# Kernel optimization log

Hardware: AMD Instinct MI355X
Metric: run time of the kernel (lower is better)

## Reference

```python
import jax, jax.numpy as jnp
import numpy as np

N_NODES = 150000       # original nodes
N_FRAG_NODES = 300000  # nodes duplicated across fragments
N_FRAGS = 30000        # number of fragments (segments of fragments_batch)
E = 1200000            # edges in combined fragment graph
D = 128                # nhid


def seg_mean(x, seg, num):
    s = jax.ops.segment_sum(x, seg, num_segments=num)
    c = jax.ops.segment_sum(jnp.ones((x.shape[0], 1), x.dtype), seg, num_segments=num)
    return s / jnp.maximum(c, 1.0)


def setup_inputs() -> dict:
    key = jax.random.key(0)
    ks = jax.random.split(key, 8)
    x = jax.random.normal(ks[0], (N_NODES, D), dtype=jnp.float32)
    mapper = jax.random.randint(ks[1], (N_FRAG_NODES,), 0, N_NODES)
    batch = jnp.sort(jax.random.randint(ks[2], (N_FRAG_NODES,), 0, N_FRAGS))
    edge_index = jax.random.randint(ks[3], (2, E), 0, N_FRAG_NODES)
    W_u = jax.random.normal(ks[4], (D, D), dtype=jnp.float32) * 0.05
    b_u = jnp.zeros((D,), dtype=jnp.float32)
    W_gcn = jax.random.normal(ks[5], (D, D), dtype=jnp.float32) * 0.05
    b_gcn = jnp.zeros((D,), dtype=jnp.float32)
    return {
        "x": x,
        "fragments_nodes_mapper": mapper,
        "fragments_batch": batch,
        "edge_index": edge_index,
        "W_u": W_u,
        "b_u": b_u,
        "W_gcn": W_gcn,
        "b_gcn": b_gcn,
        "i": 0,
    }


def gcn_conv(x, edge_index, W, b, n):
    # PyG GCNConv: add self loops, symmetric normalization D^-1/2 (A+I) D^-1/2, then linear.
    xw = x @ W  # [n, D]
    loops = jnp.arange(n, dtype=edge_index.dtype)
    row = jnp.concatenate([edge_index[0], loops])  # source
    col = jnp.concatenate([edge_index[1], loops])  # target (aggregation index)
    deg = jax.ops.segment_sum(jnp.ones(row.shape[0], x.dtype), col, num_segments=n)
    dinv = jnp.where(deg > 0, jax.lax.rsqrt(jnp.maximum(deg, 1.0)), 0.0)
    norm = dinv[row] * dinv[col]  # [E+n]
    msg = xw[row] * norm[:, None]
    out = jax.ops.segment_sum(msg, col, num_segments=n)
    return out + b


def reference(x, fragments_nodes_mapper, fragments_batch, edge_index, W_u, b_u, W_gcn, b_gcn, i):
    if i == 0:
        x = x[fragments_nodes_mapper]  # gather: [N_FRAG_NODES, D]
    # fragment-level mean pooling, broadcast back to fragment-nodes
    fragment = seg_mean(x, fragments_batch, N_FRAGS)[fragments_batch]
    # U[i-1]: MLP(nhid, nhid, nlayer=1, with_final_activation=True) -> Linear + ReLU
    x = x + jax.nn.relu(fragment @ W_u + b_u)
    # pool duplicated fragment-nodes back onto original nodes, then re-broadcast
    x = seg_mean(x, fragments_nodes_mapper, N_NODES)[fragments_nodes_mapper]
    # GCN over the combined fragment graph
    x = gcn_conv(x, edge_index, W_gcn, b_gcn, N_FRAG_NODES)
    fragment_x = seg_mean(x, fragments_batch, N_FRAGS)  # [N_FRAGS, D]
    return (fragment_x, x)
```

## Files before the change

kernel.cpp:

```cpp
#include <hip/hip_runtime.h>
#include <hip/hip_bf16.h>

#define N_NODES      150000
#define N_FRAG_NODES 300000
#define N_FRAGS      30000
#define NEDGE        1200000
#define NCNT         (N_NODES + N_FRAG_NODES)
#define D            128
#define DV           32
#define NX16         (N_NODES * 16)
#define SCAN_TILE    1024

typedef __attribute__((ext_vector_type(8))) short short8;
typedef __attribute__((ext_vector_type(8))) unsigned short u16x8;
typedef __attribute__((ext_vector_type(4))) float f32x4;
typedef __attribute__((ext_vector_type(2))) int i32x2;

__device__ __forceinline__ unsigned short f2bf(float f) {
    unsigned u = __float_as_uint(f);
    u = (u + 0x7FFFu + ((u >> 16) & 1u)) >> 16;
    return (unsigned short)u;
}
__device__ __forceinline__ float bf2f(unsigned short u) {
    return __uint_as_float((unsigned)u << 16);
}

__global__ void k_prep(const int* __restrict__ mapper, const int* __restrict__ batch,
                       const int* __restrict__ ecol, const float4* __restrict__ x4,
                       int* __restrict__ mcnt, int* __restrict__ ccnt,
                       int* __restrict__ startb, u16x8* __restrict__ x16) {
    int i = blockIdx.x * blockDim.x + threadIdx.x;
    if (i < NEDGE) atomicAdd(&ccnt[ecol[i]], 1);
    if (i < N_FRAG_NODES) atomicAdd(&mcnt[mapper[i]], 1);
    if (i <= N_FRAGS) {
        int lo = 0, hi = N_FRAG_NODES;
        while (lo < hi) { int mid = (lo + hi) >> 1; if (batch[mid] < i) lo = mid + 1; else hi = mid; }
        startb[i] = lo;
    }
    #pragma unroll
    for (int rep = 0; rep < 2; ++rep) {
        int slot = i + rep * NEDGE;
        if (slot < NX16) {
            float4 v0 = x4[(size_t)slot * 2];
            float4 v1 = x4[(size_t)slot * 2 + 1];
            u16x8 o;
            o[0] = f2bf(v0.x); o[1] = f2bf(v0.y); o[2] = f2bf(v0.z); o[3] = f2bf(v0.w);
            o[4] = f2bf(v1.x); o[5] = f2bf(v1.y); o[6] = f2bf(v1.z); o[7] = f2bf(v1.w);
            x16[slot] = o;
        }
    }
}

__global__ void k_scan_tile(const int* __restrict__ cnt, int* __restrict__ combst,
                            int* __restrict__ tsum) {
    __shared__ int buf[SCAN_TILE];
    int tid = threadIdx.x;
    int i = blockIdx.x * SCAN_TILE + tid;
    int v = (i < NCNT) ? cnt[i] : 0;
    buf[tid] = v;
    __syncthreads();
    for (int off = 1; off < SCAN_TILE; off <<= 1) {
        int t = (tid >= off) ? buf[tid - off] : 0;
        __syncthreads();
        buf[tid] += t;
        __syncthreads();
    }
    if (i < NCNT) combst[i] = buf[tid] - v;
    if (tid == SCAN_TILE - 1) tsum[blockIdx.x] = buf[tid];
}

__global__ void k_scan_tsum(int* __restrict__ tsum, int ntiles,
                            int* __restrict__ mstart, int* __restrict__ cstart) {
    __shared__ int buf[SCAN_TILE];
    int tid = threadIdx.x;
    int v = (tid < ntiles) ? tsum[tid] : 0;
    buf[tid] = v;
    __syncthreads();
    for (int off = 1; off < SCAN_TILE; off <<= 1) {
        int t = (tid >= off) ? buf[tid - off] : 0;
        __syncthreads();
        buf[tid] += t;
        __syncthreads();
    }
    if (tid < ntiles) tsum[tid] = buf[tid] - v;
    if (tid == SCAN_TILE - 1) {
        mstart[N_NODES] = N_FRAG_NODES;
        cstart[N_FRAG_NODES] = buf[tid] - N_FRAG_NODES;
    }
}

__global__ void k_scan_add(const int* __restrict__ combst, const int* __restrict__ tsum,
                           int* __restrict__ mstart, int* __restrict__ cstart,
                           const int* __restrict__ mapper, const int* __restrict__ cnt,
                           int2* __restrict__ sval) {
    int i = blockIdx.x * blockDim.x + threadIdx.x;
    if (i >= NCNT) return;
    int v = combst[i] + tsum[i >> 10];
    if (i < N_NODES) {
        mstart[i] = v;
    } else {
        int r = i - N_NODES;
        cstart[r] = v - N_FRAG_NODES;
        int2 s;
        s.x = mapper[r];
        s.y = __float_as_int(rsqrtf((float)(cnt[i] + 1)));
        sval[r] = s;
    }
}

__global__ void k_frag_mean(const u16x8* __restrict__ x16, const int* __restrict__ mapper,
                            const int* __restrict__ startb, u16x8* __restrict__ frag16) {
    int g = threadIdx.x >> 4, lane = threadIdx.x & 15;
    int b = blockIdx.x * 16 + g;
    if (b >= N_FRAGS) return;
    int s = startb[b], e = startb[b + 1];
    float a0[8], a1[8], a2[8], a3[8];
    #pragma unroll
    for (int j = 0; j < 8; ++j) { a0[j] = 0.f; a1[j] = 0.f; a2[j] = 0.f; a3[j] = 0.f; }
    int j = s;
    for (; j + 4 <= e; j += 4) {
        int m0 = mapper[j], m1 = mapper[j + 1], m2 = mapper[j + 2], m3 = mapper[j + 3];
        u16x8 v0 = x16[(size_t)m0 * 16 + lane];
        u16x8 v1 = x16[(size_t)m1 * 16 + lane];
        u16x8 v2 = x16[(size_t)m2 * 16 + lane];
        u16x8 v3 = x16[(size_t)m3 * 16 + lane];
        #pragma unroll
        for (int k = 0; k < 8; ++k) {
            a0[k] += bf2f(v0[k]); a1[k] += bf2f(v1[k]);
            a2[k] += bf2f(v2[k]); a3[k] += bf2f(v3[k]);
        }
    }
    for (; j < e; ++j) {
        int m0 = mapper[j];
        u16x8 v0 = x16[(size_t)m0 * 16 + lane];
        #pragma unroll
        for (int k = 0; k < 8; ++k) a0[k] += bf2f(v0[k]);
    }
    float c = (float)(e - s); if (c < 1.f) c = 1.f;
    float inv = 1.f / c;
    u16x8 r;
    #pragma unroll
    for (int k = 0; k < 8; ++k)
        r[k] = f2bf(((a0[k] + a1[k]) + (a2[k] + a3[k])) * inv);
    frag16[(size_t)b * 16 + lane] = r;
}

__global__ void k_build_wfrag(const float* __restrict__ W, short* __restrict__ wfrag) {
    int t = threadIdx.x;
    for (int e = t; e < 2048; e += 256) {
        int nt = e >> 8;
        int kk = (e >> 6) & 3;
        int lane = e & 63;
        int col = nt * 16 + (lane & 15);
        int kb = kk * 32 + ((lane >> 4) << 3);
        short8 v;
        #pragma unroll
        for (int j = 0; j < 8; ++j) v[j] = (short)f2bf(W[(kb + j) * D + col]);
        ((short8*)wfrag)[e] = v;
    }
}

template <bool RELU, bool BIAS>
__global__ void __launch_bounds__(256)
k_rowmat_mfma(const unsigned short* __restrict__ src16, const short* __restrict__ wfrag,
              const float* __restrict__ bias, unsigned short* __restrict__ dst16, int rows) {
    __shared__ short8 wl[2048];
    int tid = threadIdx.x;
    for (int e = tid; e < 2048; e += 256) wl[e] = ((const short8*)wfrag)[e];
    __syncthreads();
    int wv = tid >> 6, lane = tid & 63;
    int lrow = lane & 15;
    int lk8 = (lane >> 4);
    float bv[8];
    #pragma unroll
    for (int nt = 0; nt < 8; ++nt) bv[nt] = BIAS ? bias[nt * 16 + lrow] : 0.f;

    int chunk = blockIdx.x * 64;
    {
        int r = chunk + wv * 16 + lrow;
        short8 af[4];
        if (r < rows) {
            const short8* rowp = (const short8*)(src16 + (size_t)r * D);
            #pragma unroll
            for (int kk = 0; kk < 4; ++kk) af[kk] = rowp[kk * 4 + lk8];
        } else {
            #pragma unroll
            for (int kk = 0; kk < 4; ++kk) af[kk] = (short8)0;
        }
        f32x4 acc[8];
        #pragma unroll
        for (int nt = 0; nt < 8; ++nt) acc[nt] = (f32x4)0.f;
        #pragma unroll
        for (int nt = 0; nt < 8; ++nt) {
            #pragma unroll
            for (int kk = 0; kk < 4; ++kk)
                acc[nt] = __builtin_amdgcn_mfma_f32_16x16x32_bf16(
                              af[kk], wl[(nt * 4 + kk) * 64 + lane], acc[nt], 0, 0, 0);
        }
        int orow0 = chunk + wv * 16 + ((lane >> 4) << 2);
        #pragma unroll
        for (int nt = 0; nt < 8; ++nt) {
            int col = nt * 16 + lrow;
            #pragma unroll
            for (int reg = 0; reg < 4; ++reg) {
                int orow = orow0 + reg;
                if (orow < rows) {
                    float v = acc[nt][reg] + bv[nt];
                    if (RELU) v = fmaxf(v, 0.f);
                    dst16[(size_t)orow * D + col] = f2bf(v);
                }
            }
        }
    }
}

__global__ void k_fill(const int* __restrict__ mapper, const int* __restrict__ batch,
                       const int* __restrict__ erow, const int* __restrict__ ecol,
                       const int* __restrict__ mstart, int* __restrict__ mcnt,
                       int* __restrict__ mvals, const int* __restrict__ cstart,
                       int* __restrict__ ccnt, const int2* __restrict__ sval,
                       int2* __restrict__ erecs) {
    int i = blockIdx.x * blockDim.x + threadIdx.x;
    if (i < N_FRAG_NODES) {
        int k = mapper[i];
        int pos = atomicSub(&mcnt[k], 1) - 1;
        mvals[mstart[k] + pos] = batch[i];
    }
    if (i < NEDGE) {
        int c = ecol[i], r = erow[i];
        int pos = atomicSub(&ccnt[c], 1) - 1;
        erecs[cstart[c] + pos] = sval[r];
    }
}

__global__ void k_pool_csr(const u16x8* __restrict__ x16, const u16x8* __restrict__ fragu8,
                           const int* __restrict__ mstart, const int* __restrict__ mvals,
                           u16x8* __restrict__ pooled8) {
    int g = threadIdx.x >> 4, lane = threadIdx.x & 15;
    int n = blockIdx.x * 16 + g;
    if (n >= N_NODES) return;
    int s = mstart[n], e = mstart[n + 1];
    u16x8 out = (u16x8)0;
    if (e > s) {
        float accA[8], accB[8];
        #pragma unroll
        for (int j = 0; j < 8; ++j) { accA[j] = 0.f; accB[j] = 0.f; }
        int t = s;
        for (; t + 2 <= e; t += 2) {
            int b0 = mvals[t], b1 = mvals[t + 1];
            u16x8 u0 = fragu8[(size_t)b0 * 16 + lane];
            u16x8 u1 = fragu8[(size_t)b1 * 16 + lane];
            #pragma unroll
            for (int j = 0; j < 8; ++j) {
                accA[j] += bf2f(u0[j]);
                accB[j] += bf2f(u1[j]);
            }
        }
        if (t < e) {
            int b0 = mvals[t];
            u16x8 u0 = fragu8[(size_t)b0 * 16 + lane];
            #pragma unroll
            for (int j = 0; j < 8; ++j) accA[j] += bf2f(u0[j]);
        }
        float inv = 1.f / (float)(e - s);
        u16x8 xv = x16[(size_t)n * 16 + lane];
        #pragma unroll
        for (int j = 0; j < 8; ++j)
            out[j] = f2bf(fmaf(accA[j] + accB[j], inv, bf2f(xv[j])));
    }
    pooled8[(size_t)n * 16 + lane] = out;
}

__global__ void k_gcn_gather(const int* __restrict__ cstart, const int2* __restrict__ sval,
                             const int2* __restrict__ erecs, const u16x8* __restrict__ pw8,
                             const float* __restrict__ bgcn, f32x4* __restrict__ xout4) {
    int g = threadIdx.x >> 4, lane = threadIdx.x & 15;
    int c = blockIdx.x * 16 + g;
    if (c >= N_FRAG_NODES) return;
    int s = cstart[c], e = cstart[c + 1];
    int2 sv = sval[c];
    float dc = __int_as_float(sv.y);
    float acc0[8], acc1[8], acc2[8], acc3[8];
    #pragma unroll
    for (int j = 0; j < 8; ++j) { acc0[j] = 0.f; acc1[j] = 0.f; acc2[j] = 0.f; acc3[j] = 0.f; }
    int t = s;
    for (; t + 4 <= e; t += 4) {
        int2 r0 = erecs[t];
        int2 r1 = erecs[t + 1];
        int2 r2 = erecs[t + 2];
        int2 r3 = erecs[t + 3];
        u16x8 u0 = pw8[(size_t)r0.x * 16 + lane];
        u16x8 u1 = pw8[(size_t)r1.x * 16 + lane];
        u16x8 u2 = pw8[(size_t)r2.x * 16 + lane];
        u16x8 u3 = pw8[(size_t)r3.x * 16 + lane];
        float w0 = __int_as_float(r0.y), w1 = __int_as_float(r1.y);
        float w2 = __int_as_float(r2.y), w3 = __int_as_float(r3.y);
        #pragma unroll
        for (int j = 0; j < 8; ++j) {
            acc0[j] = fmaf(bf2f(u0[j]), w0, acc0[j]);
            acc1[j] = fmaf(bf2f(u1[j]), w1, acc1[j]);
            acc2[j] = fmaf(bf2f(u2[j]), w2, acc2[j]);
            acc3[j] = fmaf(bf2f(u3[j]), w3, acc3[j]);
        }
    }
    for (; t < e; ++t) {
        int2 r0 = erecs[t];
        u16x8 u0 = pw8[(size_t)r0.x * 16 + lane];
        float w0 = __int_as_float(r0.y);
        #pragma unroll
        for (int j = 0; j < 8; ++j) acc0[j] = fmaf(bf2f(u0[j]), w0, acc0[j]);
    }
    u16x8 su = pw8[(size_t)sv.x * 16 + lane];
    float dc2 = dc * dc;
    const float4* bg4 = (const float4*)bgcn;
    float4 b0 = bg4[lane * 2], b1 = bg4[lane * 2 + 1];
    float o[8];
    #pragma unroll
    for (int j = 0; j < 8; ++j)
        o[j] = fmaf((acc0[j] + acc1[j]) + (acc2[j] + acc3[j]), dc, bf2f(su[j]) * dc2);
    f32x4 o0 = {o[0] + b0.x, o[1] + b0.y, o[2] + b0.z, o[3] + b0.w};
    f32x4 o1 = {o[4] + b1.x, o[5] + b1.y, o[6] + b1.z, o[7] + b1.w};
    __builtin_nontemporal_store(o0, &xout4[(size_t)c * DV + lane * 2]);
    __builtin_nontemporal_store(o1, &xout4[(size_t)c * DV + lane * 2 + 1]);
}

__global__ void k_frag_x(const float4* __restrict__ x4, const int* __restrict__ startb,
                         float4* __restrict__ fout4) {
    int g = threadIdx.x >> 5, lane = threadIdx.x & 31;
    int b = blockIdx.x * 8 + g;
    if (b >= N_FRAGS) return;
    int s = startb[b], e = startb[b + 1];
    float4 sA = {0.f, 0.f, 0.f, 0.f}, sB = {0.f, 0.f, 0.f, 0.f};
    int j = s;
    for (; j + 2 <= e; j += 2) {
        float4 v0 = x4[(size_t)j * DV + lane];
        float4 v1 = x4[(size_t)(j + 1) * DV + lane];
        sA.x += v0.x; sA.y += v0.y; sA.z += v0.z; sA.w += v0.w;
        sB.x += v1.x; sB.y += v1.y; sB.z += v1.z; sB.w += v1.w;
    }
    if (j < e) {
        float4 v0 = x4[(size_t)j * DV + lane];
        sA.x += v0.x; sA.y += v0.y; sA.z += v0.z; sA.w += v0.w;
    }
    float4 r = {0.f, 0.f, 0.f, 0.f};
    if (e > s) {
        float inv = 1.f / (float)(e - s);
        r.x = (sA.x + sB.x) * inv; r.y = (sA.y + sB.y) * inv;
        r.z = (sA.z + sB.z) * inv; r.w = (sA.w + sB.w) * inv;
    }
    fout4[(size_t)b * DV + lane] = r;
}

extern "C" void kernel_launch(void* const* d_in, const int* in_sizes, int n_in,
                              void* d_out, int out_size, void* d_ws, size_t ws_size,
                              hipStream_t stream) {
    const float* x      = (const float*)d_in[0];
    const int*   mapper = (const int*)d_in[1];
    const int*   batch  = (const int*)d_in[2];
    const int*   erow   = (const int*)d_in[3];
    const int*   ecol   = erow + NEDGE;
    const float* W_u    = (const float*)d_in[4];
    const float* b_u    = (const float*)d_in[5];
    const float* W_gcn  = (const float*)d_in[6];
    const float* b_gcn  = (const float*)d_in[7];

    float* fout = (float*)d_out;
    float* xout = fout + (size_t)N_FRAGS * D;

    short*  wfragU   = (short*)d_ws;
    short*  wfragG   = wfragU + 16384;
    int2*   erecs    = (int2*)(wfragG + 16384);
    int2*   sval     = erecs + NEDGE;
    unsigned short* x16      = (unsigned short*)(sval + N_FRAG_NODES);
    unsigned short* frag16   = x16 + (size_t)N_NODES * D;
    unsigned short* pooled16 = frag16 + (size_t)N_FRAGS * D;
    int*    startb = (int*)(pooled16 + (size_t)N_NODES * D);
    int*    mstart = startb + (N_FRAGS + 1);
    int*    cstart = mstart + (N_NODES + 1);
    int*    mcnt   = cstart + (N_FRAG_NODES + 1);
    int*    ccnt   = mcnt + N_NODES;
    int*    mvals  = ccnt + N_FRAG_NODES;
    int*    combst = mvals + N_FRAG_NODES;
    int*    tsum   = combst + NCNT;

    hipMemsetAsync(mcnt, 0, (size_t)NCNT * sizeof(int), stream);

    k_build_wfrag<<<1, 256, 0, stream>>>(W_u, wfragU);
    k_build_wfrag<<<1, 256, 0, stream>>>(W_gcn, wfragG);

    k_prep<<<(NEDGE + 255) / 256, 256, 0, stream>>>(mapper, batch, ecol, (const float4*)x,
                                                    mcnt, ccnt, startb, (u16x8*)x16);

    int ntiles = (NCNT + SCAN_TILE - 1) / SCAN_TILE;
    k_scan_tile<<<ntiles, SCAN_TILE, 0, stream>>>(mcnt, combst, tsum);
    k_scan_tsum<<<1, SCAN_TILE, 0, stream>>>(tsum, ntiles, mstart, cstart);
    k_scan_add<<<(NCNT + 255) / 256, 256, 0, stream>>>(combst, tsum, mstart, cstart,
                                                       mapper, mcnt, sval);

    k_frag_mean<<<(N_FRAGS + 15) / 16, 256, 0, stream>>>((const u16x8*)x16, mapper, startb,
                                                         (u16x8*)frag16);
    k_rowmat_mfma<true, true><<<(N_FRAGS + 63) / 64, 256, 0, stream>>>(
        frag16, wfragU, b_u, frag16, N_FRAGS);

    k_fill<<<(NEDGE + 255) / 256, 256, 0, stream>>>(mapper, batch, erow, ecol,
                                                    mstart, mcnt, mvals,
                                                    cstart, ccnt, sval, erecs);

    k_pool_csr<<<(N_NODES + 15) / 16, 256, 0, stream>>>((const u16x8*)x16, (const u16x8*)frag16,
                                                        mstart, mvals, (u16x8*)pooled16);
    k_rowmat_mfma<false, false><<<(N_NODES + 63) / 64, 256, 0, stream>>>(
        pooled16, wfragG, nullptr, pooled16, N_NODES);

    k_gcn_gather<<<(N_FRAG_NODES + 15) / 16, 256, 0, stream>>>(cstart, sval, erecs,
                                                               (const u16x8*)pooled16,
                                                               b_gcn, (f32x4*)xout);
    k_frag_x<<<(N_FRAGS + 7) / 8, 256, 0, stream>>>((const float4*)xout, startb, (float4*)fout);
}
```

Before: 360.4 us.

## Fuse segment-mean gathers with MFMA matmuls via swizzled LDS staging

Fuses the fragment-mean gather with the W_u MFMA matmul, and the node pooling gather with the W_gcn matmul. Each block now stages its 64 pooled rows in XOR-swizzled shared memory instead of writing bf16 intermediates to global memory and reading them back. Weight-fragment building moves into k_prep to drop two tiny launches, and the k_frag_x reduction is unrolled to four accumulators. The cost is fewer rows in flight per block during the gather phase and a barrier before the MFMA phase, which may hurt latency hiding.

Result: slower. 372.4 us (+3.3%).

```diff
diff --git a/kernel.cpp b/kernel.cpp
--- a/kernel.cpp
+++ b/kernel.cpp
@@ -14,7 +14,6 @@
 typedef __attribute__((ext_vector_type(8))) short short8;
 typedef __attribute__((ext_vector_type(8))) unsigned short u16x8;
 typedef __attribute__((ext_vector_type(4))) float f32x4;
-typedef __attribute__((ext_vector_type(2))) int i32x2;
 
 __device__ __forceinline__ unsigned short f2bf(float f) {
     unsigned u = __float_as_uint(f);
@@ -27,8 +26,10 @@
 
 __global__ void k_prep(const int* __restrict__ mapper, const int* __restrict__ batch,
                        const int* __restrict__ ecol, const float4* __restrict__ x4,
+                       const float* __restrict__ W_u, const float* __restrict__ W_gcn,
                        int* __restrict__ mcnt, int* __restrict__ ccnt,
-                       int* __restrict__ startb, u16x8* __restrict__ x16) {
+                       int* __restrict__ startb, u16x8* __restrict__ x16,
+                       short* __restrict__ wfragU, short* __restrict__ wfragG) {
     int i = blockIdx.x * blockDim.x + threadIdx.x;
     if (i < NEDGE) atomicAdd(&ccnt[ecol[i]], 1);
     if (i < N_FRAG_NODES) atomicAdd(&mcnt[mapper[i]], 1);
@@ -36,6 +37,20 @@
         int lo = 0, hi = N_FRAG_NODES;
         while (lo < hi) { int mid = (lo + hi) >> 1; if (batch[mid] < i) lo = mid + 1; else hi = mid; }
         startb[i] = lo;
+    }
+    if (i < 4096) {
+        const float* W = (i < 2048) ? W_u : W_gcn;
+        short* wf = (i < 2048) ? wfragU : wfragG;
+        int e = i & 2047;
+        int nt = e >> 8;
+        int kk = (e >> 6) & 3;
+        int lane = e & 63;
+        int col = nt * 16 + (lane & 15);
+        int kb = kk * 32 + ((lane >> 4) << 3);
+        short8 v;
+        #pragma unroll
+        for (int j = 0; j < 8; ++j) v[j] = (short)f2bf(W[(kb + j) * D + col]);
+        ((short8*)wf)[e] = v;
     }
     #pragma unroll
     for (int rep = 0; rep < 2; ++rep) {
@@ -108,110 +123,92 @@
     }
 }
 
-__global__ void k_frag_mean(const u16x8* __restrict__ x16, const int* __restrict__ mapper,
-                            const int* __restrict__ startb, u16x8* __restrict__ frag16) {
-    int g = threadIdx.x >> 4, lane = threadIdx.x & 15;
-    int b = blockIdx.x * 16 + g;
-    if (b >= N_FRAGS) return;
-    int s = startb[b], e = startb[b + 1];
-    float a0[8], a1[8], a2[8], a3[8];
-    #pragma unroll
-    for (int j = 0; j < 8; ++j) { a0[j] = 0.f; a1[j] = 0.f; a2[j] = 0.f; a3[j] = 0.f; }
-    int j = s;
-    for (; j + 4 <= e; j += 4) {
-        int m0 = mapper[j], m1 = mapper[j + 1], m2 = mapper[j + 2], m3 = mapper[j + 3];
-        u16x8 v0 = x16[(size_t)m0 * 16 + lane];
-        u16x8 v1 = x16[(size_t)m1 * 16 + lane];
-        u16x8 v2 = x16[(size_t)m2 * 16 + lane];
-        u16x8 v3 = x16[(size_t)m3 * 16 + lane];
-        #pragma unroll
-        for (int k = 0; k < 8; ++k) {
-            a0[k] += bf2f(v0[k]); a1[k] += bf2f(v1[k]);
-            a2[k] += bf2f(v2[k]); a3[k] += bf2f(v3[k]);
-        }
-    }
-    for (; j < e; ++j) {
-        int m0 = mapper[j];
-        u16x8 v0 = x16[(size_t)m0 * 16 + lane];
-        #pragma unroll
-        for (int k = 0; k < 8; ++k) a0[k] += bf2f(v0[k]);
-    }
-    float c = (float)(e - s); if (c < 1.f) c = 1.f;
-    float inv = 1.f / c;
-    u16x8 r;
-    #pragma unroll
-    for (int k = 0; k < 8; ++k)
-        r[k] = f2bf(((a0[k] + a1[k]) + (a2[k] + a3[k])) * inv);
-    frag16[(size_t)b * 16 + lane] = r;
-}
-
-__global__ void k_build_wfrag(const float* __restrict__ W, short* __restrict__ wfrag) {
-    int t = threadIdx.x;
-    for (int e = t; e < 2048; e += 256) {
-        int nt = e >> 8;
-        int kk = (e >> 6) & 3;
-        int lane = e & 63;
-        int col = nt * 16 + (lane & 15);
-        int kb = kk * 32 + ((lane >> 4) << 3);
-        short8 v;
-        #pragma unroll
-        for (int j = 0; j < 8; ++j) v[j] = (short)f2bf(W[(kb + j) * D + col]);
-        ((short8*)wfrag)[e] = v;
-    }
-}
-
 template <bool RELU, bool BIAS>
-__global__ void __launch_bounds__(256)
-k_rowmat_mfma(const unsigned short* __restrict__ src16, const short* __restrict__ wfrag,
-              const float* __restrict__ bias, unsigned short* __restrict__ dst16, int rows) {
-    __shared__ short8 wl[2048];
-    int tid = threadIdx.x;
-    for (int e = tid; e < 2048; e += 256) wl[e] = ((const short8*)wfrag)[e];
-    __syncthreads();
+__device__ __forceinline__ void mfma_phase(const short8* __restrict__ wl,
+                                           const short8* __restrict__ stage,
+                                           const float* __restrict__ bias,
+                                           unsigned short* __restrict__ dst16,
+                                           int chunk, int rows, int tid) {
     int wv = tid >> 6, lane = tid & 63;
     int lrow = lane & 15;
     int lk8 = (lane >> 4);
-    float bv[8];
-    #pragma unroll
-    for (int nt = 0; nt < 8; ++nt) bv[nt] = BIAS ? bias[nt * 16 + lrow] : 0.f;
-
-    int chunk = blockIdx.x * 64;
-    {
-        int r = chunk + wv * 16 + lrow;
-        short8 af[4];
-        if (r < rows) {
-            const short8* rowp = (const short8*)(src16 + (size_t)r * D);
-            #pragma unroll
-            for (int kk = 0; kk < 4; ++kk) af[kk] = rowp[kk * 4 + lk8];
-        } else {
-            #pragma unroll
-            for (int kk = 0; kk < 4; ++kk) af[kk] = (short8)0;
-        }
-        f32x4 acc[8];
-        #pragma unroll
-        for (int nt = 0; nt < 8; ++nt) acc[nt] = (f32x4)0.f;
-        #pragma unroll
-        for (int nt = 0; nt < 8; ++nt) {
-            #pragma unroll
-            for (int kk = 0; kk < 4; ++kk)
-                acc[nt] = __builtin_amdgcn_mfma_f32_16x16x32_bf16(
-                              af[kk], wl[(nt * 4 + kk) * 64 + lane], acc[nt], 0, 0, 0);
-        }
-        int orow0 = chunk + wv * 16 + ((lane >> 4) << 2);
-        #pragma unroll
-        for (int nt = 0; nt < 8; ++nt) {
-            int col = nt * 16 + lrow;
-            #pragma unroll
-            for (int reg = 0; reg < 4; ++reg) {
-                int orow = orow0 + reg;
-                if (orow < rows) {
-                    float v = acc[nt][reg] + bv[nt];
-                    if (RELU) v = fmaxf(v, 0.f);
-                    dst16[(size_t)orow * D + col] = f2bf(v);
-                }
+    int r16 = wv * 16 + lrow;
+    short8 af[4];
+    #pragma unroll
+    for (int kk = 0; kk < 4; ++kk)
+        af[kk] = stage[r16 * 16 + (((kk << 2) + lk8) ^ (r16 & 7))];
+    f32x4 acc[8];
+    #pragma unroll
+    for (int nt = 0; nt < 8; ++nt) acc[nt] = (f32x4)0.f;
+    #pragma unroll
+    for (int nt = 0; nt < 8; ++nt) {
+        #pragma unroll
+        for (int kk = 0; kk < 4; ++kk)
+            acc[nt] = __builtin_amdgcn_mfma_f32_16x16x32_bf16(
+                          af[kk], wl[(nt * 4 + kk) * 64 + lane], acc[nt], 0, 0, 0);
+    }
+    int orow0 = chunk + wv * 16 + ((lane >> 4) << 2);
+    #pragma unroll
+    for (int nt = 0; nt < 8; ++nt) {
+        int col = nt * 16 + lrow;
+        float bv = BIAS ? bias[col] : 0.f;
+        #pragma unroll
+        for (int reg = 0; reg < 4; ++reg) {
+            int orow = orow0 + reg;
+            if (orow < rows) {
+                float v = acc[nt][reg] + bv;
+                if (RELU) v = fmaxf(v, 0.f);
+                dst16[(size_t)orow * D + col] = f2bf(v);
             }
         }
     }
+}
+
+__global__ void __launch_bounds__(256)
+k_frag_mm(const u16x8* __restrict__ x16, const int* __restrict__ mapper,
+          const int* __restrict__ startb, const short* __restrict__ wfragU,
+          const float* __restrict__ b_u, unsigned short* __restrict__ fragu16) {
+    __shared__ short8 wl[2048];
+    __shared__ short8 stage[1024];
+    int tid = threadIdx.x;
+    for (int e = tid; e < 2048; e += 256) wl[e] = ((const short8*)wfragU)[e];
+    int g = tid >> 4, lane = tid & 15;
+    int chunk = blockIdx.x * 64;
+    #pragma unroll
+    for (int nn = 0; nn < 4; ++nn) {
+        int r = nn * 16 + g;
+        int b = chunk + r;
+        u16x8 out = (u16x8)0;
+        if (b < N_FRAGS) {
+            int s = startb[b], e = startb[b + 1];
+            float a0[8], a1[8];
+            #pragma unroll
+            for (int j = 0; j < 8; ++j) { a0[j] = 0.f; a1[j] = 0.f; }
+            int j = s;
+            for (; j + 2 <= e; j += 2) {
+                int m0 = mapper[j], m1 = mapper[j + 1];
+                u16x8 v0 = x16[(size_t)m0 * 16 + lane];
+                u16x8 v1 = x16[(size_t)m1 * 16 + lane];
+                #pragma unroll
+                for (int k = 0; k < 8; ++k) { a0[k] += bf2f(v0[k]); a1[k] += bf2f(v1[k]); }
+            }
+            if (j < e) {
+                u16x8 v0 = x16[(size_t)mapper[j] * 16 + lane];
+                #pragma unroll
+                for (int k = 0; k < 8; ++k) a0[k] += bf2f(v0[k]);
+            }
+            float c = (float)(e - s); if (c < 1.f) c = 1.f;
+            float inv = 1.f / c;
+            #pragma unroll
+            for (int k = 0; k < 8; ++k) out[k] = f2bf((a0[k] + a1[k]) * inv);
+        }
+        short8 o;
+        #pragma unroll
+        for (int k = 0; k < 8; ++k) o[k] = (short)out[k];
+        stage[r * 16 + (lane ^ (r & 7))] = o;
+    }
+    __syncthreads();
+    mfma_phase<true, true>(wl, stage, b_u, fragu16, chunk, N_FRAGS, tid);
 }
 
 __global__ void k_fill(const int* __restrict__ mapper, const int* __restrict__ batch,
@@ -233,42 +230,54 @@
     }
 }
 
-__global__ void k_pool_csr(const u16x8* __restrict__ x16, const u16x8* __restrict__ fragu8,
-                           const int* __restrict__ mstart, const int* __restrict__ mvals,
-                           u16x8* __restrict__ pooled8) {
-    int g = threadIdx.x >> 4, lane = threadIdx.x & 15;
-    int n = blockIdx.x * 16 + g;
-    if (n >= N_NODES) return;
-    int s = mstart[n], e = mstart[n + 1];
-    u16x8 out = (u16x8)0;
-    if (e > s) {
-        float accA[8], accB[8];
-        #pragma unroll
-        for (int j = 0; j < 8; ++j) { accA[j] = 0.f; accB[j] = 0.f; }
-        int t = s;
-        for (; t + 2 <= e; t += 2) {
-            int b0 = mvals[t], b1 = mvals[t + 1];
-            u16x8 u0 = fragu8[(size_t)b0 * 16 + lane];
-            u16x8 u1 = fragu8[(size_t)b1 * 16 + lane];
-            #pragma unroll
-            for (int j = 0; j < 8; ++j) {
-                accA[j] += bf2f(u0[j]);
-                accB[j] += bf2f(u1[j]);
+__global__ void __launch_bounds__(256)
+k_pool_mm(const u16x8* __restrict__ x16, const u16x8* __restrict__ fragu8,
+          const int* __restrict__ mstart, const int* __restrict__ mvals,
+          const short* __restrict__ wfragG, unsigned short* __restrict__ pw16) {
+    __shared__ short8 wl[2048];
+    __shared__ short8 stage[1024];
+    int tid = threadIdx.x;
+    for (int e = tid; e < 2048; e += 256) wl[e] = ((const short8*)wfragG)[e];
+    int g = tid >> 4, lane = tid & 15;
+    int chunk = blockIdx.x * 64;
+    #pragma unroll
+    for (int nn = 0; nn < 4; ++nn) {
+        int r = nn * 16 + g;
+        int n = chunk + r;
+        u16x8 out = (u16x8)0;
+        if (n < N_NODES) {
+            int s = mstart[n], e = mstart[n + 1];
+            if (e > s) {
+                float a0[8], a1[8];
+                #pragma unroll
+                for (int j = 0; j < 8; ++j) { a0[j] = 0.f; a1[j] = 0.f; }
+                int t = s;
+                for (; t + 2 <= e; t += 2) {
+                    int b0 = mvals[t], b1 = mvals[t + 1];
+                    u16x8 u0 = fragu8[(size_t)b0 * 16 + lane];
+                    u16x8 u1 = fragu8[(size_t)b1 * 16 + lane];
+                    #pragma unroll
+                    for (int j = 0; j < 8; ++j) { a0[j] += bf2f(u0[j]); a1[j] += bf2f(u1[j]); }
+                }
+                if (t < e) {
+                    u16x8 u0 = fragu8[(size_t)mvals[t] * 16 + lane];
+                    #pragma unroll
+                    for (int j = 0; j < 8; ++j) a0[j] += bf2f(u0[j]);
+                }
+                float inv = 1.f / (float)(e - s);
+                u16x8 xv = x16[(size_t)n * 16 + lane];
+                #pragma unroll
+                for (int j = 0; j < 8; ++j)
+                    out[j] = f2bf(fmaf(a0[j] + a1[j], inv, bf2f(xv[j])));
             }
         }
-        if (t < e) {
-            int b0 = mvals[t];
-            u16x8 u0 = fragu8[(size_t)b0 * 16 + lane];
-            #pragma unroll
-            for (int j = 0; j < 8; ++j) accA[j] += bf2f(u0[j]);
-        }
-        float inv = 1.f / (float)(e - s);
-        u16x8 xv = x16[(size_t)n * 16 + lane];
-        #pragma unroll
-        for (int j = 0; j < 8; ++j)
-            out[j] = f2bf(fmaf(accA[j] + accB[j], inv, bf2f(xv[j])));
-    }
-    pooled8[(size_t)n * 16 + lane] = out;
+        short8 o;
+        #pragma unroll
+        for (int k = 0; k < 8; ++k) o[k] = (short)out[k];
+        stage[r * 16 + (lane ^ (r & 7))] = o;
+    }
+    __syncthreads();
+    mfma_phase<false, false>(wl, stage, nullptr, pw16, chunk, N_NODES, tid);
 }
 
 __global__ void k_gcn_gather(const int* __restrict__ cstart, const int2* __restrict__ sval,
@@ -330,23 +339,30 @@
     int b = blockIdx.x * 8 + g;
     if (b >= N_FRAGS) return;
     int s = startb[b], e = startb[b + 1];
-    float4 sA = {0.f, 0.f, 0.f, 0.f}, sB = {0.f, 0.f, 0.f, 0.f};
+    float4 s0 = {0.f,0.f,0.f,0.f}, s1 = {0.f,0.f,0.f,0.f};
+    float4 s2 = {0.f,0.f,0.f,0.f}, s3 = {0.f,0.f,0.f,0.f};
     int j = s;
-    for (; j + 2 <= e; j += 2) {
+    for (; j + 4 <= e; j += 4) {
         float4 v0 = x4[(size_t)j * DV + lane];
         float4 v1 = x4[(size_t)(j + 1) * DV + lane];
-        sA.x += v0.x; sA.y += v0.y; sA.z += v0.z; sA.w += v0.w;
-        sB.x += v1.x; sB.y += v1.y; sB.z += v1.z; sB.w += v1.w;
-    }
-    if (j < e) {
+        float4 v2 = x4[(size_t)(j + 2) * DV + lane];
+        float4 v3 = x4[(size_t)(j + 3) * DV + lane];
+        s0.x += v0.x; s0.y += v0.y; s0.z += v0.z; s0.w += v0.w;
+        s1.x += v1.x; s1.y += v1.y; s1.z += v1.z; s1.w += v1.w;
+        s2.x += v2.x; s2.y += v2.y; s2.z += v2.z; s2.w += v2.w;
+        s3.x += v3.x; s3.y += v3.y; s3.z += v3.z; s3.w += v3.w;
+    }
+    for (; j < e; ++j) {
         float4 v0 = x4[(size_t)j * DV + lane];
-        sA.x += v0.x; sA.y += v0.y; sA.z += v0.z; sA.w += v0.w;
+        s0.x += v0.x; s0.y += v0.y; s0.z += v0.z; s0.w += v0.w;
     }
     float4 r = {0.f, 0.f, 0.f, 0.f};
     if (e > s) {
         float inv = 1.f / (float)(e - s);
-        r.x = (sA.x + sB.x) * inv; r.y = (sA.y + sB.y) * inv;
-        r.z = (sA.z + sB.z) * inv; r.w = (sA.w + sB.w) * inv;
+        r.x = ((s0.x + s1.x) + (s2.x + s3.x)) * inv;
+        r.y = ((s0.y + s1.y) + (s2.y + s3.y)) * inv;
+        r.z = ((s0.z + s1.z) + (s2.z + s3.z)) * inv;
+        r.w = ((s0.w + s1.w) + (s2.w + s3.w)) * inv;
     }
     fout4[(size_t)b * DV + lane] = r;
 }
@@ -372,9 +388,9 @@
     int2*   erecs    = (int2*)(wfragG + 16384);
     int2*   sval     = erecs + NEDGE;
     unsigned short* x16      = (unsigned short*)(sval + N_FRAG_NODES);
-    unsigned short* frag16   = x16 + (size_t)N_NODES * D;
-    unsigned short* pooled16 = frag16 + (size_t)N_FRAGS * D;
-    int*    startb = (int*)(pooled16 + (size_t)N_NODES * D);
+    unsigned short* fragu16  = x16 + (size_t)N_NODES * D;
+    unsigned short* pw16     = fragu16 + (size_t)N_FRAGS * D;
+    int*    startb = (int*)(pw16 + (size_t)N_NODES * D);
     int*    mstart = startb + (N_FRAGS + 1);
     int*    cstart = mstart + (N_NODES + 1);
     int*    mcnt   = cstart + (N_FRAG_NODES + 1);
@@ -385,11 +401,9 @@
 
     hipMemsetAsync(mcnt, 0, (size_t)NCNT * sizeof(int), stream);
 
-    k_build_wfrag<<<1, 256, 0, stream>>>(W_u, wfragU);
-    k_build_wfrag<<<1, 256, 0, stream>>>(W_gcn, wfragG);
-
     k_prep<<<(NEDGE + 255) / 256, 256, 0, stream>>>(mapper, batch, ecol, (const float4*)x,
-                                                    mcnt, ccnt, startb, (u16x8*)x16);
+                                                    W_u, W_gcn, mcnt, ccnt, startb,
+                                                    (u16x8*)x16, wfragU, wfragG);
 
     int ntiles = (NCNT + SCAN_TILE - 1) / SCAN_TILE;
     k_scan_tile<<<ntiles, SCAN_TILE, 0, stream>>>(mcnt, combst, tsum);
@@ -397,22 +411,18 @@
     k_scan_add<<<(NCNT + 255) / 256, 256, 0, stream>>>(combst, tsum, mstart, cstart,
                                                        mapper, mcnt, sval);
 
-    k_frag_mean<<<(N_FRAGS + 15) / 16, 256, 0, stream>>>((const u16x8*)x16, mapper, startb,
-                                                         (u16x8*)frag16);
-    k_rowmat_mfma<true, true><<<(N_FRAGS + 63) / 64, 256, 0, stream>>>(
-        frag16, wfragU, b_u, frag16, N_FRAGS);
+    k_frag_mm<<<(N_FRAGS + 63) / 64, 256, 0, stream>>>((const u16x8*)x16, mapper, startb,
+                                                       wfragU, b_u, fragu16);
 
     k_fill<<<(NEDGE + 255) / 256, 256, 0, stream>>>(mapper, batch, erow, ecol,
                                                     mstart, mcnt, mvals,
                                                     cstart, ccnt, sval, erecs);
 
-    k_pool_csr<<<(N_NODES + 15) / 16, 256, 0, stream>>>((const u16x8*)x16, (const u16x8*)frag16,
-                                                        mstart, mvals, (u16x8*)pooled16);
-    k_rowmat_mfma<false, false><<<(N_NODES + 63) / 64, 256, 0, stream>>>(
-        pooled16, wfragG, nullptr, pooled16, N_NODES);
+    k_pool_mm<<<(N_NODES + 63) / 64, 256, 0, stream>>>((const u16x8*)x16, (const u16x8*)fragu16,
+                                                       mstart, mvals, wfragG, pw16);
 
     k_gcn_gather<<<(N_FRAG_NODES + 15) / 16, 256, 0, stream>>>(cstart, sval, erecs,
-                                                               (const u16x8*)pooled16,
+                                                               (const u16x8*)pw16,
                                                                b_gcn, (f32x4*)xout);
     k_frag_x<<<(N_FRAGS + 7) / 8, 256, 0, stream>>>((const float4*)xout, startb, (float4*)fout);
 }
```
